# Kernel optimization log

Hardware: AMD Instinct MI355X
Metric: run time of the kernel (lower is better)

## Reference

```python
import jax, jax.numpy as jnp
import numpy as np

N = 30000
F_IN = 500
HID = 16
OUT = 3
E = 960000


def setup_inputs() -> dict:
    key = jax.random.key(0)
    ks = jax.random.split(key, 10)
    x = jax.random.normal(ks[0], (N, F_IN), dtype=jnp.float32)
    edge_index = jax.random.randint(ks[1], (2, E), 0, N, dtype=jnp.int32)
    # CNN params (torch Conv1d: weight [out, in, k], bias [out])
    s1 = 1.0 / np.sqrt(1 * 3)
    s2 = 1.0 / np.sqrt(HID * 3)
    conv1_w = jax.random.uniform(ks[2], (HID, 1, 3), jnp.float32, -s1, s1)
    conv1_b = jax.random.uniform(ks[3], (HID,), jnp.float32, -s1, s1)
    conv2_w = jax.random.uniform(ks[4], (HID, HID, 3), jnp.float32, -s2, s2)
    conv2_b = jax.random.uniform(ks[5], (HID,), jnp.float32, -s2, s2)
    # GCNConv params (glorot weight [in, out], zero bias)
    g1 = np.sqrt(6.0 / (HID + HID))
    g2 = np.sqrt(6.0 / (HID + OUT))
    gcn1_w = jax.random.uniform(ks[6], (HID, HID), jnp.float32, -g1, g1)
    gcn1_b = jnp.zeros((HID,), jnp.float32)
    gcn2_w = jax.random.uniform(ks[7], (HID, OUT), jnp.float32, -g2, g2)
    gcn2_b = jnp.zeros((OUT,), jnp.float32)
    return {"x": x, "conv1_w": conv1_w, "conv1_b": conv1_b,
            "conv2_w": conv2_w, "conv2_b": conv2_b,
            "gcn1_w": gcn1_w, "gcn1_b": gcn1_b,
            "gcn2_w": gcn2_w, "gcn2_b": gcn2_b,
            "edge_index": edge_index}


def _conv1d(x, w, b):
    # x: [N, C_in, L], w: [C_out, C_in, 3], padding=1
    y = jax.lax.conv_general_dilated(
        x, w, window_strides=(1,), padding=[(1, 1)],
        dimension_numbers=("NCH", "OIH", "NCH"))
    return y + b[None, :, None]


def _gcn_conv(x, w, b, src, dst, n):
    # x: [n, d_in] -> [n, d_out]; Kipf normalization with self-loops
    h = x @ w
    loop = jnp.arange(n, dtype=src.dtype)
    s = jnp.concatenate([src, loop])
    d = jnp.concatenate([dst, loop])
    deg = jax.ops.segment_sum(jnp.ones_like(d, dtype=h.dtype), d, num_segments=n)
    dinv = jnp.where(deg > 0, jax.lax.rsqrt(deg), 0.0)
    norm = dinv[s] * dinv[d]                      # [E+n]
    msg = h[s] * norm[:, None]                    # gather + scale
    return jax.ops.segment_sum(msg, d, num_segments=n) + b


def reference(x, conv1_w, conv1_b, conv2_w, conv2_b,
              gcn1_w, gcn1_b, gcn2_w, gcn2_b, edge_index):
    # CNN feature extractor over feature axis
    h = x[:, None, :]                             # [N, 1, F_IN]
    h = jax.nn.relu(_conv1d(h, conv1_w, conv1_b))  # [N, HID, F_IN]
    h = jax.nn.relu(_conv1d(h, conv2_w, conv2_b))  # [N, HID, F_IN]
    h = jnp.max(h, axis=2)                        # global max pool -> [N, HID]
    # GCN
    src, dst = edge_index[0], edge_index[1]
    n = h.shape[0]
    h = jax.nn.relu(_gcn_conv(h, gcn1_w, gcn1_b, src, dst, n))
    h = _gcn_conv(h, gcn2_w, gcn2_b, src, dst, n)  # [N, OUT]
    return jax.nn.log_softmax(h, axis=1)
```

## Files before the change

### kernel.cpp

```cpp
#include <hip/hip_runtime.h>
#include <hip/hip_bf16.h>

#define N_NODES 30000
#define F_INLEN 500
#define HID 16
#define OUTC 3
#define NEDGE 960000
#define YPITCH 20
#define NBIN 938
#define HBLK 128
#define EPRH (NEDGE / HBLK)
#define ECAP 1536
#define NPB2 235

typedef float  f32x4 __attribute__((ext_vector_type(4)));
typedef float  f32x2 __attribute__((ext_vector_type(2)));
typedef short  s16x8 __attribute__((ext_vector_type(8)));

static __device__ __forceinline__ unsigned short f2bf(float f) {
    unsigned int u = __float_as_uint(f);
    unsigned int r = (u + 0x7fffu + ((u >> 16) & 1u)) >> 16;
    return (unsigned short)r;
}
static __device__ __forceinline__ unsigned int pack_bf16x2(float v0, float v1) {
#if __has_builtin(__builtin_amdgcn_cvt_pk_bf16_f32)
    typedef __bf16 bf16x2_t __attribute__((ext_vector_type(2)));
    union { bf16x2_t v; unsigned int u; } cv;
    cv.v = __builtin_amdgcn_cvt_pk_bf16_f32(v0, v1);
    return cv.u;
#else
    return __builtin_amdgcn_perm(__float_as_uint(v1), __float_as_uint(v0), 0x07060302);
#endif
}

__global__ void setup_kernel(const float* __restrict__ w2, short* __restrict__ bfragsG,
                             int* __restrict__ degi)
{
    const int tid = threadIdx.x;
    const int gid = blockIdx.x * 256 + tid;
    if (gid < N_NODES) degi[gid] = 0;
    if (blockIdx.x == 0 && tid < 64) {
        const int n16 = tid & 15, q = tid >> 4;
#pragma unroll
        for (int j = 0; j < 8; j++) {
            {
                const int c = q * 8 + j;
                const int t = c >> 4, i = c & 15;
                bfragsG[tid * 16 + j] = (short)f2bf(w2[n16 * 48 + i * 3 + t]);
            }
            {
                const int c = 32 + q * 8 + j;
                short v = 0;
                if (c < 48) { const int t = c >> 4, i = c & 15; v = (short)f2bf(w2[n16 * 48 + i * 3 + t]); }
                bfragsG[tid * 16 + 8 + j] = v;
            }
        }
    }
}

__global__ __launch_bounds__(256, 7) void conv_hist(
    const float* __restrict__ x,
    const float* __restrict__ w1, const float* __restrict__ b1,
    const float* __restrict__ b2, const short* __restrict__ bfragsG,
    const int* __restrict__ dst, int* __restrict__ degi,
    int* __restrict__ cntbase, float* __restrict__ h0)
{
    __shared__ __align__(16) float xp[502];
    __shared__ __align__(16) unsigned short yh[516 * YPITCH];
    __shared__ float red[64];

    const int tid = threadIdx.x;

    if (blockIdx.x < HBLK) {
        int* histH = (int*)yh;
        for (int i = tid; i < NBIN; i += 256) histH[i] = 0;
        __syncthreads();
        const int e0 = blockIdx.x * EPRH;
        for (int e = e0 + tid; e < e0 + EPRH; e += 256) {
            const int d = dst[e];
            atomicAdd(&histH[d >> 5], 1);
            atomicAdd(&degi[d], 1);
        }
        __syncthreads();
        for (int i = tid; i < NBIN; i += 256) cntbase[i * HBLK + blockIdx.x] = histH[i];
        return;
    }

    const int node = blockIdx.x - HBLK;
    const int lane = tid & 63;
    const int wave = tid >> 6;
    const int n16  = lane & 15;
    const int q    = lane >> 4;

    if (tid == 0) { xp[0] = 0.f; xp[501] = 0.f; }
    if (tid < 125) {
        const float4 v = ((const float4*)(x + (long long)node * F_INLEN))[tid];
        xp[4 * tid + 1] = v.x; xp[4 * tid + 2] = v.y;
        xp[4 * tid + 3] = v.z; xp[4 * tid + 4] = v.w;
    }
    {
        const int ri = tid >> 4;
        const int row = (ri == 0) ? 0 : (500 + ri);
        yh[row * YPITCH + (tid & 15)] = 0;
    }
    const s16x8* bfp = (const s16x8*)(bfragsG + lane * 16);
    const s16x8 bh0 = bfp[0], bh1 = bfp[1];

    f32x2 wt0[8], wt1[8], wt2[8], bb[8];
#pragma unroll
    for (int cp = 0; cp < 8; cp++) {
        const int c0 = 2 * cp, c1 = 2 * cp + 1;
        wt0[cp] = (f32x2){w1[c0 * 3 + 0], w1[c1 * 3 + 0]};
        wt1[cp] = (f32x2){w1[c0 * 3 + 1], w1[c1 * 3 + 1]};
        wt2[cp] = (f32x2){w1[c0 * 3 + 2], w1[c1 * 3 + 2]};
        bb[cp]  = (f32x2){b1[c0], b1[c1]};
    }
    __syncthreads();

    for (int p = tid; p < 500; p += 256) {
        const float x0 = xp[p], x1 = xp[p + 1], x2 = xp[p + 2];
        const f32x2 xv0 = {x0, x0}, xv1 = {x1, x1}, xv2 = {x2, x2};
        const f32x2 zero = {0.f, 0.f};
        unsigned int hp[8];
#pragma unroll
        for (int cp = 0; cp < 8; cp++) {
            f32x2 a = bb[cp];
            a = __builtin_elementwise_fma(wt0[cp], xv0, a);
            a = __builtin_elementwise_fma(wt1[cp], xv1, a);
            a = __builtin_elementwise_fma(wt2[cp], xv2, a);
            a = __builtin_elementwise_max(a, zero);
            hp[cp] = pack_bf16x2(a[0], a[1]);
        }
        uint2* d = (uint2*)&yh[(p + 1) * YPITCH];
        d[0] = make_uint2(hp[0], hp[1]);
        d[1] = make_uint2(hp[2], hp[3]);
        d[2] = make_uint2(hp[4], hp[5]);
        d[3] = make_uint2(hp[6], hp[7]);
    }
    __syncthreads();

    struct S8 { short4 lo, hi; };
    float mx0 = -3.0e38f, mx1 = -3.0e38f, mx2 = -3.0e38f, mx3 = -3.0e38f;
#pragma unroll
    for (int it = 0; it < 8; it++) {
        const int tile = wave * 8 + it;
        const int p0 = tile * 16 + n16;
        const int cA = (q & 1) * 8;
        const int rA = p0 + (q >> 1);
        const int rB = p0 + 2 + (q >> 1);
        S8 t0, t1;
        t0.lo = *(const short4*)&yh[rA * YPITCH + cA];
        t0.hi = *(const short4*)&yh[rA * YPITCH + cA + 4];
        t1.lo = *(const short4*)&yh[rB * YPITCH + cA];
        t1.hi = *(const short4*)&yh[rB * YPITCH + cA + 4];
        const s16x8 ah0 = *(const s16x8*)&t0;
        const s16x8 ah1 = *(const s16x8*)&t1;
        f32x4 acc = {0.f, 0.f, 0.f, 0.f};
        acc = __builtin_amdgcn_mfma_f32_16x16x32_bf16(ah0, bh0, acc, 0, 0, 0);
        acc = __builtin_amdgcn_mfma_f32_16x16x32_bf16(ah1, bh1, acc, 0, 0, 0);
        if (it < 7) {
            mx0 = fmaxf(mx0, acc[0]);
            mx1 = fmaxf(mx1, acc[1]);
            mx2 = fmaxf(mx2, acc[2]);
            mx3 = fmaxf(mx3, acc[3]);
        } else if (wave < 3) {
            mx0 = fmaxf(mx0, acc[0]);
            mx1 = fmaxf(mx1, acc[1]);
            mx2 = fmaxf(mx2, acc[2]);
            mx3 = fmaxf(mx3, acc[3]);
        } else if (q == 0) {
            mx0 = fmaxf(mx0, acc[0]);
            mx1 = fmaxf(mx1, acc[1]);
            mx2 = fmaxf(mx2, acc[2]);
            mx3 = fmaxf(mx3, acc[3]);
        }
    }
    float m = fmaxf(fmaxf(mx0, mx1), fmaxf(mx2, mx3));
    m = fmaxf(m, __shfl_xor(m, 16));
    m = fmaxf(m, __shfl_xor(m, 32));
    if (lane < 16) red[wave * 16 + lane] = m;
    __syncthreads();
    if (tid < 16) {
        const float mm = fmaxf(fmaxf(red[tid], red[16 + tid]), fmaxf(red[32 + tid], red[48 + tid]));
        h0[node * HID + tid] = fmaxf(mm + b2[tid], 0.f);
    }
}

__global__ __launch_bounds__(512) void reorder2(
    const int* __restrict__ src, const int* __restrict__ dst,
    const int* __restrict__ cntbase, int* __restrict__ packed,
    int* __restrict__ binstart, const int* __restrict__ degi,
    float* __restrict__ dinv)
{
    __shared__ int scA[NBIN], scB[NBIN];
    __shared__ int gexc[NBIN];
    __shared__ int lexc[NBIN];
    __shared__ int cursor[NBIN];
    __shared__ int srt[EPRH];
    __shared__ unsigned short sbin[EPRH];
    const int tid = threadIdx.x;
    const int blk = blockIdx.x;

    const int kblk = blk >> 2, rem = blk & 3;
    for (int bin = tid; bin < NBIN; bin += 512) {
        const int4* row = (const int4*)(cntbase + bin * HBLK);
        int tot = 0, psum = 0, lc = 0;
        for (int k = 0; k < kblk; k++) {
            const int4 v = row[k];
            const int s4 = v.x + v.y + v.z + v.w;
            tot += s4; psum += s4;
        }
        {
            const int4 v = row[kblk];
            tot += v.x + v.y + v.z + v.w;
            if (rem > 0) psum += v.x;
            if (rem > 1) psum += v.y;
            if (rem > 2) psum += v.z;
            lc = (rem == 0) ? v.x : (rem == 1) ? v.y : (rem == 2) ? v.z : v.w;
        }
        for (int k = kblk + 1; k < HBLK / 4; k++) {
            const int4 v = row[k];
            tot += v.x + v.y + v.z + v.w;
        }
        cursor[bin] = tot;
        gexc[bin]   = psum;
        lexc[bin]   = lc;
        scA[bin]    = tot;
    }
    __syncthreads();
    {
        int* pA = scA; int* pB = scB;
        for (int off = 1; off < NBIN; off <<= 1) {
            for (int i = tid; i < NBIN; i += 512)
                pB[i] = pA[i] + ((i >= off) ? pA[i - off] : 0);
            __syncthreads();
            int* tp = pA; pA = pB; pB = tp;
        }
        for (int i = tid; i < NBIN; i += 512) {
            const int excl = pA[i] - cursor[i];
            gexc[i] += excl;
            if (blk == 0) binstart[i] = excl;
        }
        if (blk == 0 && tid == 0) binstart[NBIN] = NEDGE;
    }
    __syncthreads();
    for (int i = tid; i < NBIN; i += 512) scA[i] = lexc[i];
    __syncthreads();
    {
        int* pA = scA; int* pB = scB;
        for (int off = 1; off < NBIN; off <<= 1) {
            for (int i = tid; i < NBIN; i += 512)
                pB[i] = pA[i] + ((i >= off) ? pA[i - off] : 0);
            __syncthreads();
            int* tp = pA; pA = pB; pB = tp;
        }
        for (int i = tid; i < NBIN; i += 512) {
            const int e2 = pA[i] - lexc[i];
            lexc[i] = e2;
            cursor[i] = e2;
        }
    }
    __syncthreads();
    const int e0 = blk * EPRH;
    for (int e = e0 + tid; e < e0 + EPRH; e += 512) {
        const int d = dst[e];
        const int bin = d >> 5;
        const int pos = atomicAdd(&cursor[bin], 1);
        srt[pos] = src[e] | ((d & 31) << 16);
        sbin[pos] = (unsigned short)bin;
    }
    __syncthreads();
    for (int i = tid; i < EPRH; i += 512) {
        const int bin = sbin[i];
        packed[gexc[bin] + (i - lexc[bin])] = srt[i];
    }
    const int n0 = blk * NPB2;
    for (int n = n0 + tid; n < n0 + NPB2 && n < N_NODES; n += 512)
        dinv[n] = rsqrtf((float)(degi[n] + 1));
}

__global__ __launch_bounds__(256) void agg1_kernel(
    const int* __restrict__ binstart, const int* __restrict__ packed,
    const float* __restrict__ h0, const float* __restrict__ dinv,
    const float* __restrict__ W1, const float* __restrict__ b1g,
    const float* __restrict__ W2, float4* __restrict__ t2p4)
{
    __shared__ float w1s[256];
    __shared__ float w2s[48];
    __shared__ float b1s[16];
    __shared__ float accS[32 * 17];
    __shared__ int eL[ECAP];
    __shared__ int srt[ECAP];
    __shared__ int h32[32], ls32[32], lofs32[32];
    const int tid = threadIdx.x;
    const int blk = blockIdx.x;
    w1s[tid] = W1[tid];
    if (tid < 48) w2s[tid] = W2[tid];
    if (tid < 16) b1s[tid] = b1g[tid];
    if (tid < 32) h32[tid] = 0;
    const int beg = binstart[blk];
    const int cnt = binstart[blk + 1] - beg;
    __syncthreads();
    for (int j = tid; j < cnt; j += 256) {
        const int p = packed[beg + j];
        eL[j] = p;
        atomicAdd(&h32[p >> 16], 1);
    }
    __syncthreads();
    if (tid < 32) {
        const int v = h32[tid];
        int inc = v;
#pragma unroll
        for (int off = 1; off < 32; off <<= 1) {
            const int y = __shfl_up(inc, off);
            if (tid >= off) inc += y;
        }
        ls32[tid] = inc - v;
        lofs32[tid] = inc - v;
    }
    __syncthreads();
    for (int j = tid; j < cnt; j += 256) {
        const int p = eL[j];
        const int pos = atomicAdd(&lofs32[p >> 16], 1);
        srt[pos] = p;
    }
    __syncthreads();
    const int n = tid >> 3;
    const int eslot = (tid >> 2) & 1;
    const int q = tid & 3;
    const int node = blk * 32 + n;
    const bool valid = node < N_NODES;
    f32x4 acc = {0.f, 0.f, 0.f, 0.f};
    if (valid) {
        const int s0 = ls32[n];
        const int s1 = s0 + h32[n];
        for (int i = s0 + eslot; i < s1; i += 2) {
            const int s = srt[i] & 0xFFFF;
            const f32x4 v = *(const f32x4*)(h0 + s * HID + q * 4);
            acc += v * dinv[s];
        }
    }
#pragma unroll
    for (int c = 0; c < 4; c++) acc[c] += __shfl_xor(acc[c], 4);
    if (valid && eslot == 0) {
        const f32x4 sf = *(const f32x4*)(h0 + node * HID + q * 4);
        acc += sf * dinv[node];
        accS[n * 17 + q * 4 + 0] = acc[0];
        accS[n * 17 + q * 4 + 1] = acc[1];
        accS[n * 17 + q * 4 + 2] = acc[2];
        accS[n * 17 + q * 4 + 3] = acc[3];
    }
    __syncthreads();
    if (tid < 128) {
        const int n2 = tid >> 2;
        const int node2 = blk * 32 + n2;
        if (node2 < N_NODES) {
            const float dv = dinv[node2];
            const int q2 = tid & 3;
            float y0 = 0.f, y1 = 0.f, y2 = 0.f, y3 = 0.f;
#pragma unroll
            for (int i = 0; i < 16; i++) {
                const float a = accS[n2 * 17 + i];
                y0 = fmaf(a, w1s[i * 16 + q2 * 4 + 0], y0);
                y1 = fmaf(a, w1s[i * 16 + q2 * 4 + 1], y1);
                y2 = fmaf(a, w1s[i * 16 + q2 * 4 + 2], y2);
                y3 = fmaf(a, w1s[i * 16 + q2 * 4 + 3], y3);
            }
            float d0 = 0.f, d1 = 0.f, d2 = 0.f;
            const float yv[4] = {y0, y1, y2, y3};
#pragma unroll
            for (int j = 0; j < 4; j++) {
                const int o = q2 * 4 + j;
                const float h = fmaxf(b1s[o] + dv * yv[j], 0.f);
                d0 = fmaf(h, w2s[o * 3 + 0], d0);
                d1 = fmaf(h, w2s[o * 3 + 1], d1);
                d2 = fmaf(h, w2s[o * 3 + 2], d2);
            }
            d0 += __shfl_xor(d0, 1); d0 += __shfl_xor(d0, 2);
            d1 += __shfl_xor(d1, 1); d1 += __shfl_xor(d1, 2);
            d2 += __shfl_xor(d2, 1); d2 += __shfl_xor(d2, 2);
            if (q2 == 0) t2p4[node2] = make_float4(d0 * dv, d1 * dv, d2 * dv, 0.f);
        }
    }
}

__global__ __launch_bounds__(256) void agg2_kernel(
    const int* __restrict__ binstart, const int* __restrict__ packed,
    const float4* __restrict__ t2p4, const float* __restrict__ dinv,
    const float* __restrict__ b2g, float* __restrict__ out)
{
    __shared__ int eL[ECAP];
    __shared__ int srt[ECAP];
    __shared__ int h32[32], ls32[32], lofs32[32];
    const int tid = threadIdx.x;
    const int blk = blockIdx.x;
    if (tid < 32) h32[tid] = 0;
    const int beg = binstart[blk];
    const int cnt = binstart[blk + 1] - beg;
    __syncthreads();
    for (int j = tid; j < cnt; j += 256) {
        const int p = packed[beg + j];
        eL[j] = p;
        atomicAdd(&h32[p >> 16], 1);
    }
    __syncthreads();
    if (tid < 32) {
        const int v = h32[tid];
        int inc = v;
#pragma unroll
        for (int off = 1; off < 32; off <<= 1) {
            const int y = __shfl_up(inc, off);
            if (tid >= off) inc += y;
        }
        ls32[tid] = inc - v;
        lofs32[tid] = inc - v;
    }
    __syncthreads();
    for (int j = tid; j < cnt; j += 256) {
        const int p = eL[j];
        const int pos = atomicAdd(&lofs32[p >> 16], 1);
        srt[pos] = p;
    }
    __syncthreads();
    const int n = tid >> 3;
    const int ln8 = tid & 7;
    const int node = blk * 32 + n;
    float a0 = 0.f, a1 = 0.f, a2 = 0.f;
    if (node < N_NODES) {
        const int s0 = ls32[n];
        const int s1 = s0 + h32[n];
        for (int i = s0 + ln8; i < s1; i += 8) {
            const int s = srt[i] & 0xFFFF;
            const float4 v = t2p4[s];
            a0 += v.x; a1 += v.y; a2 += v.z;
        }
    }
#pragma unroll
    for (int msk = 1; msk < 8; msk <<= 1) {
        a0 += __shfl_xor(a0, msk);
        a1 += __shfl_xor(a1, msk);
        a2 += __shfl_xor(a2, msk);
    }
    if (ln8 == 0 && node < N_NODES) {
        const float dv = dinv[node];
        const float4 self = t2p4[node];
        const float z0 = b2g[0] + dv * (a0 + self.x);
        const float z1 = b2g[1] + dv * (a1 + self.y);
        const float z2 = b2g[2] + dv * (a2 + self.z);
        const float m = fmaxf(z0, fmaxf(z1, z2));
        const float lg = m + logf(expf(z0 - m) + expf(z1 - m) + expf(z2 - m));
        out[node * 3 + 0] = z0 - lg;
        out[node * 3 + 1] = z1 - lg;
        out[node * 3 + 2] = z2 - lg;
    }
}

extern "C" void kernel_launch(void* const* d_in, const int* in_sizes, int n_in,
                              void* d_out, int out_size, void* d_ws, size_t ws_size,
                              hipStream_t stream)
{
    const float* x   = (const float*)d_in[0];
    const float* w1  = (const float*)d_in[1];
    const float* b1  = (const float*)d_in[2];
    const float* w2  = (const float*)d_in[3];
    const float* b2  = (const float*)d_in[4];
    const float* g1w = (const float*)d_in[5];
    const float* g1b = (const float*)d_in[6];
    const float* g2w = (const float*)d_in[7];
    const float* g2b = (const float*)d_in[8];
    const int*   ei  = (const int*)d_in[9];
    const int* src = ei;
    const int* dst = ei + NEDGE;

    float* ws = (float*)d_ws;
    float*  h0      = ws;
    float*  dinv    = ws + 480000;
    float4* t2p4    = (float4*)(ws + 510000);
    int*    degi    = (int*)(ws + 630000);
    int*    cntbase = (int*)(ws + 660000);
    int*    binstart= (int*)(ws + 780064);
    int*    packed  = (int*)(ws + 781024);
    short*  bfragsG = (short*)(ws + 1741024);
    float*  out     = (float*)d_out;

    setup_kernel<<<118, 256, 0, stream>>>(w2, bfragsG, degi);
    conv_hist<<<HBLK + N_NODES, 256, 0, stream>>>(x, w1, b1, b2, bfragsG,
                                                  dst, degi, cntbase, h0);
    reorder2<<<HBLK, 512, 0, stream>>>(src, dst, cntbase, packed, binstart, degi, dinv);
    agg1_kernel<<<NBIN, 256, 0, stream>>>(binstart, packed, h0, dinv,
                                          g1w, g1b, g2w, t2p4);
    agg2_kernel<<<NBIN, 256, 0, stream>>>(binstart, packed, t2p4, dinv, g2b, out);
}
```

Before: 228.5 us.

## Double reorder blocks, pack bin into edge word, prescale h0 by dinv

Raises the histogram/reorder block count from 128 to 256 so each reorder block handles half as many edges. It packs the full destination index into the edge word (src in 15 bits, dst shifted by 15), so the bin can be decoded from the word and the separate shared sbin array goes away. The reorder kernel now multiplies h0 rows by dinv in place, so agg1 no longer gathers dinv per edge. The risks are a larger cntbase, extra h0 read/write traffic in reorder2, and a dependence on node indices fitting in 15 bits.

After: 266.0 us. +16.4%, slower.

```diff
diff --git a/kernel.cpp b/kernel.cpp
--- a/kernel.cpp
+++ b/kernel.cpp
@@ -8,10 +8,10 @@
 #define NEDGE 960000
 #define YPITCH 20
 #define NBIN 938
-#define HBLK 128
+#define HBLK 256
 #define EPRH (NEDGE / HBLK)
 #define ECAP 1536
-#define NPB2 235
+#define NPB2 118
 
 typedef float  f32x4 __attribute__((ext_vector_type(4)));
 typedef float  f32x2 __attribute__((ext_vector_type(2)));
@@ -190,14 +190,13 @@
     const int* __restrict__ src, const int* __restrict__ dst,
     const int* __restrict__ cntbase, int* __restrict__ packed,
     int* __restrict__ binstart, const int* __restrict__ degi,
-    float* __restrict__ dinv)
+    float* __restrict__ dinv, float* __restrict__ h0)
 {
     __shared__ int scA[NBIN], scB[NBIN];
     __shared__ int gexc[NBIN];
     __shared__ int lexc[NBIN];
     __shared__ int cursor[NBIN];
     __shared__ int srt[EPRH];
-    __shared__ unsigned short sbin[EPRH];
     const int tid = threadIdx.x;
     const int blk = blockIdx.x;
 
@@ -266,17 +265,21 @@
         const int d = dst[e];
         const int bin = d >> 5;
         const int pos = atomicAdd(&cursor[bin], 1);
-        srt[pos] = src[e] | ((d & 31) << 16);
-        sbin[pos] = (unsigned short)bin;
+        srt[pos] = src[e] | (d << 15);
     }
     __syncthreads();
     for (int i = tid; i < EPRH; i += 512) {
-        const int bin = sbin[i];
+        const int bin = srt[i] >> 20;
         packed[gexc[bin] + (i - lexc[bin])] = srt[i];
     }
     const int n0 = blk * NPB2;
-    for (int n = n0 + tid; n < n0 + NPB2 && n < N_NODES; n += 512)
-        dinv[n] = rsqrtf((float)(degi[n] + 1));
+    for (int n = n0 + tid; n < n0 + NPB2 && n < N_NODES; n += 512) {
+        const float dv = rsqrtf((float)(degi[n] + 1));
+        dinv[n] = dv;
+        f32x4* h4 = (f32x4*)(h0 + n * HID);
+#pragma unroll
+        for (int k = 0; k < 4; k++) h4[k] = h4[k] * dv;
+    }
 }
 
 __global__ __launch_bounds__(256) void agg1_kernel(
@@ -304,7 +307,7 @@
     for (int j = tid; j < cnt; j += 256) {
         const int p = packed[beg + j];
         eL[j] = p;
-        atomicAdd(&h32[p >> 16], 1);
+        atomicAdd(&h32[(p >> 15) & 31], 1);
     }
     __syncthreads();
     if (tid < 32) {
@@ -321,7 +324,7 @@
     __syncthreads();
     for (int j = tid; j < cnt; j += 256) {
         const int p = eL[j];
-        const int pos = atomicAdd(&lofs32[p >> 16], 1);
+        const int pos = atomicAdd(&lofs32[(p >> 15) & 31], 1);
         srt[pos] = p;
     }
     __syncthreads();
@@ -335,16 +338,14 @@
         const int s0 = ls32[n];
         const int s1 = s0 + h32[n];
         for (int i = s0 + eslot; i < s1; i += 2) {
-            const int s = srt[i] & 0xFFFF;
-            const f32x4 v = *(const f32x4*)(h0 + s * HID + q * 4);
-            acc += v * dinv[s];
+            const int s = srt[i] & 32767;
+            acc += *(const f32x4*)(h0 + s * HID + q * 4);
         }
     }
 #pragma unroll
     for (int c = 0; c < 4; c++) acc[c] += __shfl_xor(acc[c], 4);
     if (valid && eslot == 0) {
-        const f32x4 sf = *(const f32x4*)(h0 + node * HID + q * 4);
-        acc += sf * dinv[node];
+        acc += *(const f32x4*)(h0 + node * HID + q * 4);
         accS[n * 17 + q * 4 + 0] = acc[0];
         accS[n * 17 + q * 4 + 1] = acc[1];
         accS[n * 17 + q * 4 + 2] = acc[2];
@@ -401,7 +402,7 @@
     for (int j = tid; j < cnt; j += 256) {
         const int p = packed[beg + j];
         eL[j] = p;
-        atomicAdd(&h32[p >> 16], 1);
+        atomicAdd(&h32[(p >> 15) & 31], 1);
     }
     __syncthreads();
     if (tid < 32) {
@@ -418,7 +419,7 @@
     __syncthreads();
     for (int j = tid; j < cnt; j += 256) {
         const int p = eL[j];
-        const int pos = atomicAdd(&lofs32[p >> 16], 1);
+        const int pos = atomicAdd(&lofs32[(p >> 15) & 31], 1);
         srt[pos] = p;
     }
     __syncthreads();
@@ -430,7 +431,7 @@
         const int s0 = ls32[n];
         const int s1 = s0 + h32[n];
         for (int i = s0 + ln8; i < s1; i += 8) {
-            const int s = srt[i] & 0xFFFF;
+            const int s = srt[i] & 32767;
             const float4 v = t2p4[s];
             a0 += v.x; a1 += v.y; a2 += v.z;
         }
@@ -478,15 +479,16 @@
     float4* t2p4    = (float4*)(ws + 510000);
     int*    degi    = (int*)(ws + 630000);
     int*    cntbase = (int*)(ws + 660000);
-    int*    binstart= (int*)(ws + 780064);
-    int*    packed  = (int*)(ws + 781024);
-    short*  bfragsG = (short*)(ws + 1741024);
+    int*    binstart= (int*)(ws + 900128);
+    int*    packed  = (int*)(ws + 901152);
+    short*  bfragsG = (short*)(ws + 1861152);
     float*  out     = (float*)d_out;
 
     setup_kernel<<<118, 256, 0, stream>>>(w2, bfragsG, degi);
     conv_hist<<<HBLK + N_NODES, 256, 0, stream>>>(x, w1, b1, b2, bfragsG,
                                                   dst, degi, cntbase, h0);
-    reorder2<<<HBLK, 512, 0, stream>>>(src, dst, cntbase, packed, binstart, degi, dinv);
+    reorder2<<<HBLK, 512, 0, stream>>>(src, dst, cntbase, packed, binstart,
+                                       degi, dinv, h0);
     agg1_kernel<<<NBIN, 256, 0, stream>>>(binstart, packed, h0, dinv,
                                           g1w, g1b, g2w, t2p4);
     agg2_kernel<<<NBIN, 256, 0, stream>>>(binstart, packed, t2p4, dinv, g2b, out);
```
